# Kernel tuning notes

Hardware: AMD Instinct MI355X
Metric: run time of the kernel (lower is better)

The kernel has to match this reference:

```python
import jax, jax.numpy as jnp
import numpy as np

N_NODES = 50000
N_EDGES = 800000
IN_F = 128
OUT_F = 32
HEADS = 4
EDGE_F = 32  # must equal OUT_F for the original module's shapes to broadcast


def setup_inputs() -> dict:
    key = jax.random.key(0)
    k1, k2, k3, k4, k5, k6, k7 = jax.random.split(key, 7)
    h = jax.random.normal(k1, (N_NODES, IN_F), dtype=jnp.float32)
    edge_indices = jax.random.randint(k2, (2, N_EDGES), 0, N_NODES, dtype=jnp.int32)
    edge_attr = jax.random.normal(k3, (N_EDGES, EDGE_F), dtype=jnp.float32)
    # learned parameters (xavier-ish scaling)
    W = jax.random.normal(k4, (IN_F, HEADS * OUT_F), dtype=jnp.float32) * (1.0 / np.sqrt(IN_F))
    a = jax.random.normal(k5, (HEADS, 2 * OUT_F + EDGE_F), dtype=jnp.float32) * 0.1
    eW = jax.random.normal(k6, (EDGE_F, HEADS * OUT_F), dtype=jnp.float32) * (1.0 / np.sqrt(EDGE_F))
    eb = jnp.zeros((HEADS * OUT_F,), dtype=jnp.float32)
    return {"h": h, "edge_indices": edge_indices, "edge_attr": edge_attr,
            "W": W, "a": a, "eW": eW, "eb": eb}


def reference(h, edge_indices, edge_attr, W, a, eW, eb):
    N = h.shape[0]
    H = a.shape[0]
    F = W.shape[1] // H
    row, col = edge_indices[0], edge_indices[1]

    # node / edge projections
    ht = (h @ W).reshape(N, H, F)                       # [N,H,F]
    et = (edge_attr @ eW + eb).reshape(-1, H, F)        # [E,H,F]

    # split attention vector; avoids materializing the [E,H,3F] concat
    a_i, a_j, a_e = a[:, :F], a[:, F:2 * F], a[:, 2 * F:]
    alpha_i = jnp.einsum('nhf,hf->nh', ht, a_i)         # [N,H]
    alpha_j = jnp.einsum('nhf,hf->nh', ht, a_j)         # [N,H]
    e = alpha_i[row] + alpha_j[col] + jnp.einsum('ehf,hf->eh', et, a_e)  # [E,H]
    e = jax.nn.leaky_relu(e, negative_slope=0.2)

    # scatter-softmax over edges grouped by destination (row), global-max stabilized
    e_exp = jnp.exp(e - jnp.max(e))                     # matches torch exp(e - e.max())
    denom = jax.ops.segment_sum(e_exp, row, num_segments=N)  # [N,H]
    att = e_exp / (denom[row] + 1e-8)                   # [E,H]

    # weighted scatter-add aggregation
    hj = ht[col]                                        # [E,H,F]
    h_out = jax.ops.segment_sum(att[:, :, None] * hj, row, num_segments=N)  # [N,H,F]
    h_out = h_out.reshape(N, H * F)                     # concat=True
    h_out = jax.nn.elu(h_out)                           # dropout=0 (eval)
    return h_out, att
```

## Files before the change

kernel.cpp:

```cpp
#include <hip/hip_runtime.h>
#include <hip/hip_bf16.h>
#include <hip/hip_fp16.h>

#define N_NODES 50000
#define N_EDGES 800000
#define IN_F 128
#define OUT_F 32
#define HEADS 4
#define EDGE_F 32
#define HF 128
#define NB 16
#define SB 256
#define NBLK ((N_NODES + SB - 1) / SB)


__global__ void prep_kernel(const float* __restrict__ eW, const float* __restrict__ eb,
                            const float* __restrict__ a,
                            float* __restrict__ w_eff, float* __restrict__ b_eff) {
    int t = threadIdx.x;
    if (t < 128) {
        int k = t >> 2, h = t & 3;
        float s = 0.f;
        #pragma unroll
        for (int f = 0; f < EDGE_F; ++f)
            s = fmaf(eW[k * HF + h * OUT_F + f], a[h * 96 + 2 * OUT_F + f], s);
        w_eff[k * 4 + h] = s;
    } else if (t < 132) {
        int h = t - 128;
        float s = 0.f;
        #pragma unroll
        for (int f = 0; f < EDGE_F; ++f)
            s = fmaf(eb[h * OUT_F + f], a[h * 96 + 2 * OUT_F + f], s);
        b_eff[h] = s;
    }
}

__global__ __launch_bounds__(256) void node_kernel(
        const float* __restrict__ h, const float* __restrict__ W,
        const float* __restrict__ a,
        __hip_bfloat16* __restrict__ ht_bf,
        float* __restrict__ alpha_i, float* __restrict__ alpha_j) {
    int tid = threadIdx.x;
    int g = tid >> 6, lane = tid & 63;
    int n0 = blockIdx.x * NB;
    __shared__ __align__(16) float hs[NB][IN_F];
    {
        const float4* src = (const float4*)(h + (size_t)n0 * IN_F);
        float4* dst = (float4*)(&hs[0][0]);
        dst[tid] = src[tid];
        dst[tid + 256] = src[tid + 256];
    }
    __syncthreads();
    float acc0[4] = {0.f, 0.f, 0.f, 0.f};
    float acc1[4] = {0.f, 0.f, 0.f, 0.f};
    const float2* Wv = (const float2*)W;
    #pragma unroll 8
    for (int k4 = 0; k4 < IN_F / 4; ++k4) {
        float4 hv[4];
        #pragma unroll
        for (int i = 0; i < 4; ++i)
            hv[i] = *(const float4*)&hs[g * 4 + i][k4 * 4];
        #pragma unroll
        for (int kk = 0; kk < 4; ++kk) {
            float2 w = Wv[(k4 * 4 + kk) * 64 + lane];
            #pragma unroll
            for (int i = 0; i < 4; ++i) {
                float hvv = (&hv[i].x)[kk];
                acc0[i] = fmaf(hvv, w.x, acc0[i]);
                acc1[i] = fmaf(hvv, w.y, acc1[i]);
            }
        }
    }
    int hh = lane >> 4;
    int f0 = (2 * lane) & 31;
    float ai0 = a[hh * 96 + f0],      ai1 = a[hh * 96 + f0 + 1];
    float aj0 = a[hh * 96 + 32 + f0], aj1 = a[hh * 96 + 32 + f0 + 1];
    #pragma unroll
    for (int i = 0; i < 4; ++i) {
        int n = n0 + g * 4 + i;
        *(__hip_bfloat162*)(ht_bf + (size_t)n * HF + 2 * lane) =
            __float22bfloat162_rn(make_float2(acc0[i], acc1[i]));
        float pi = fmaf(acc0[i], ai0, acc1[i] * ai1);
        float pj = fmaf(acc0[i], aj0, acc1[i] * aj1);
        #pragma unroll
        for (int s = 8; s > 0; s >>= 1) {
            pi += __shfl_down(pi, s, 16);
            pj += __shfl_down(pj, s, 16);
        }
        if ((lane & 15) == 0) {
            alpha_i[n * 4 + hh] = pi;
            alpha_j[n * 4 + hh] = pj;
        }
    }
}

__global__ __launch_bounds__(256) void count_kernel(const int* __restrict__ row,
                                                    int* __restrict__ deg,
                                                    int* __restrict__ rank) {
    int t = blockIdx.x * 256 + threadIdx.x;
    if (t < N_EDGES / 4) {
        int4 r4 = ((const int4*)row)[t];
        int4 k4;
        k4.x = atomicAdd(&deg[r4.x], 1);
        k4.y = atomicAdd(&deg[r4.y], 1);
        k4.z = atomicAdd(&deg[r4.z], 1);
        k4.w = atomicAdd(&deg[r4.w], 1);
        ((int4*)rank)[t] = k4;
    }
}

__device__ __forceinline__ int block_incl_scan(int v, int lane, int wid, int* wsum) {
    int x = v;
    #pragma unroll
    for (int s = 1; s < 64; s <<= 1) {
        int y = __shfl_up(x, s, 64);
        if (lane >= s) x += y;
    }
    if (lane == 63) wsum[wid] = x;
    __syncthreads();
    int add = 0;
    #pragma unroll
    for (int w = 0; w < 4; ++w) add += (w < wid) ? wsum[w] : 0;
    return x + add;
}

__global__ __launch_bounds__(SB) void scan1_kernel(const int* __restrict__ deg,
                                                   int* __restrict__ row_off,
                                                   int* __restrict__ blk_sums) {
    __shared__ int wsum[4];
    int i = blockIdx.x * SB + threadIdx.x;
    int v = (i < N_NODES) ? deg[i] : 0;
    int incl = block_incl_scan(v, threadIdx.x & 63, threadIdx.x >> 6, wsum);
    if (i < N_NODES) row_off[i] = incl - v;
    if (threadIdx.x == SB - 1) blk_sums[blockIdx.x] = incl;
}

__global__ __launch_bounds__(SB) void scan2_kernel(int* __restrict__ blk_sums,
                                                   int* __restrict__ blk_off,
                                                   int* __restrict__ row_off) {
    __shared__ int wsum[4];
    int t = threadIdx.x;
    int v = (t < NBLK) ? blk_sums[t] : 0;
    int incl = block_incl_scan(v, t & 63, t >> 6, wsum);
    if (t < NBLK) blk_off[t] = incl - v;
    if (t == SB - 1) row_off[N_NODES] = incl;
}

__global__ __launch_bounds__(SB) void scan3_kernel(const int* __restrict__ blk_off,
                                                   int* __restrict__ row_off) {
    int i = blockIdx.x * SB + threadIdx.x;
    if (i < N_NODES)
        row_off[i] += blk_off[blockIdx.x];
}

__global__ __launch_bounds__(256) void edge_kernel(
        const int* __restrict__ row, const int* __restrict__ col,
        const float* __restrict__ ea,
        const float* __restrict__ w_eff, const float* __restrict__ b_eff,
        const float* __restrict__ alpha_i, const float* __restrict__ alpha_j,
        const int* __restrict__ row_off, const int* __restrict__ rank,
        uint4* __restrict__ rec) {
    __shared__ float wsd[128];
    __shared__ float bs[4];
    int t = threadIdx.x;
    if (t < 128) wsd[t] = w_eff[t];
    if (t < 4) bs[t] = b_eff[t];
    __syncthreads();
    int e = blockIdx.x * 256 + t;
    const float4* src = (const float4*)(ea + (size_t)e * EDGE_F);
    float4 ev[8];
    #pragma unroll
    for (int i = 0; i < 8; ++i) ev[i] = src[i];
    int r = row[e], c = col[e];
    int rk = rank[e];
    float4 ai = *(const float4*)(alpha_i + (size_t)r * 4);
    float4 aj = *(const float4*)(alpha_j + (size_t)c * 4);
    float s0 = bs[0], s1 = bs[1], s2 = bs[2], s3 = bs[3];
    #pragma unroll
    for (int i = 0; i < 8; ++i) {
        #pragma unroll
        for (int kk = 0; kk < 4; ++kk) {
            float x = (&ev[i].x)[kk];
            float4 w4 = *(const float4*)&wsd[(i * 4 + kk) * 4];
            s0 = fmaf(x, w4.x, s0);
            s1 = fmaf(x, w4.y, s1);
            s2 = fmaf(x, w4.z, s2);
            s3 = fmaf(x, w4.w, s3);
        }
    }
    float e0 = s0 + ai.x + aj.x;
    float e1 = s1 + ai.y + aj.y;
    float e2 = s2 + ai.z + aj.z;
    float e3 = s3 + ai.w + aj.w;
    e0 = e0 > 0.f ? e0 : 0.2f * e0;
    e1 = e1 > 0.f ? e1 : 0.2f * e1;
    e2 = e2 > 0.f ? e2 : 0.2f * e2;
    e3 = e3 > 0.f ? e3 : 0.2f * e3;
    __half2 p01 = __floats2half2_rn(__expf(e0), __expf(e1));
    __half2 p23 = __floats2half2_rn(__expf(e2), __expf(e3));
    uint4 out;
    out.x = *reinterpret_cast<unsigned int*>(&p01);
    out.y = *reinterpret_cast<unsigned int*>(&p23);
    out.z = (unsigned int)c;
    out.w = (unsigned int)e;
    int pos = row_off[r] + rk;
    rec[pos] = out;
}

__global__ __launch_bounds__(256) void agg_kernel(
        const int* __restrict__ row_off, const uint4* __restrict__ rec,
        const __hip_bfloat16* __restrict__ ht_bf,
        float* __restrict__ hout, float* __restrict__ att) {
    int wave = threadIdx.x >> 6;
    int lane = threadIdx.x & 63;
    int n = blockIdx.x * 4 + wave;
    if (n >= N_NODES) return;
    int beg = row_off[n], end = row_off[n + 1];
    int h2 = lane >> 4;
    int sh = (h2 & 1) * 16;
    float2 acc0 = {0.f, 0.f}, acc1 = {0.f, 0.f};
    float den0 = 0.f, den1 = 0.f;
    int p = beg;
    for (; p + 1 < end; p += 2) {
        uint4 rA = rec[p];
        uint4 rB = rec[p + 1];
        unsigned int wA = (h2 & 2) ? rA.y : rA.x;
        unsigned int wB = (h2 & 2) ? rB.y : rB.x;
        float exA = __half2float(__ushort_as_half((unsigned short)(wA >> sh)));
        float exB = __half2float(__ushort_as_half((unsigned short)(wB >> sh)));
        int cA = (int)rA.z;
        int cB = (int)rB.z;
        float2 hvA = __bfloat1622float2(
            *(const __hip_bfloat162*)(ht_bf + (size_t)cA * HF + 2 * lane));
        float2 hvB = __bfloat1622float2(
            *(const __hip_bfloat162*)(ht_bf + (size_t)cB * HF + 2 * lane));
        acc0.x = fmaf(exA, hvA.x, acc0.x); acc0.y = fmaf(exA, hvA.y, acc0.y);
        acc1.x = fmaf(exB, hvB.x, acc1.x); acc1.y = fmaf(exB, hvB.y, acc1.y);
        den0 += exA; den1 += exB;
    }
    if (p < end) {
        uint4 rA = rec[p];
        unsigned int wA = (h2 & 2) ? rA.y : rA.x;
        float exA = __half2float(__ushort_as_half((unsigned short)(wA >> sh)));
        int cA = (int)rA.z;
        float2 hvA = __bfloat1622float2(
            *(const __hip_bfloat162*)(ht_bf + (size_t)cA * HF + 2 * lane));
        acc0.x = fmaf(exA, hvA.x, acc0.x); acc0.y = fmaf(exA, hvA.y, acc0.y);
        den0 += exA;
    }
    float den = den0 + den1;
    float rden = 1.0f / (den + 1e-8f);
    float ox = (acc0.x + acc1.x) * rden, oy = (acc0.y + acc1.y) * rden;
    ox = ox > 0.f ? ox : expm1f(ox);
    oy = oy > 0.f ? oy : expm1f(oy);
    float2 o = {ox, oy};
    ((float2*)(hout + (size_t)n * HF))[lane] = o;
    int h = lane & 3;
    float rden_h = __shfl(rden, h * 16, 64);
    for (int p0 = beg; p0 < end; p0 += 16) {
        int q = p0 + (lane >> 2);
        if (q < end) {
            uint4 rQ = rec[q];
            unsigned int w = (h & 2) ? rQ.y : rQ.x;
            float ex = __half2float(__ushort_as_half((unsigned short)(w >> ((h & 1) * 16))));
            att[(size_t)rQ.w * 4 + h] = ex * rden_h;
        }
    }
}

extern "C" void kernel_launch(void* const* d_in, const int* in_sizes, int n_in,
                              void* d_out, int out_size, void* d_ws, size_t ws_size,
                              hipStream_t stream) {
    const float* h  = (const float*)d_in[0];
    const int*   ei = (const int*)  d_in[1];
    const float* ea = (const float*)d_in[2];
    const float* W  = (const float*)d_in[3];
    const float* a  = (const float*)d_in[4];
    const float* eW = (const float*)d_in[5];
    const float* eb = (const float*)d_in[6];

    float* out  = (float*)d_out;
    float* hout = out;
    float* att  = out + (size_t)N_NODES * HF;

    char* wsb = (char*)d_ws;
    __hip_bfloat16* ht_bf = (__hip_bfloat16*)wsb;
    float* alpha_i = (float*)(wsb + (size_t)N_NODES * HF * 2);
    float* alpha_j = alpha_i + N_NODES * HEADS;
    float* w_eff   = alpha_j + N_NODES * HEADS;
    float* b_eff   = w_eff + 128;
    int*   deg     = (int*)(b_eff + 4);
    int*   row_off = deg + N_NODES;
    int*   blk_sums= row_off + N_NODES + 1;
    int*   blk_off = blk_sums + NBLK;
    int*   rank    = (int*)((((uintptr_t)(blk_off + NBLK)) + 15) & ~(uintptr_t)15);
    uint4* rec     = (uint4*)((((uintptr_t)(rank + N_EDGES)) + 15) & ~(uintptr_t)15);

    const int* row = ei;
    const int* col = ei + N_EDGES;

    hipMemsetAsync(deg, 0, (size_t)N_NODES * sizeof(int), stream);

    prep_kernel<<<1, 160, 0, stream>>>(eW, eb, a, w_eff, b_eff);
    node_kernel<<<N_NODES / NB, 256, 0, stream>>>(h, W, a, ht_bf, alpha_i, alpha_j);
    count_kernel<<<(N_EDGES / 4 + 255) / 256, 256, 0, stream>>>(row, deg, rank);
    scan1_kernel<<<NBLK, SB, 0, stream>>>(deg, row_off, blk_sums);
    scan2_kernel<<<1, SB, 0, stream>>>(blk_sums, blk_off, row_off);
    scan3_kernel<<<NBLK, SB, 0, stream>>>(blk_off, row_off);
    edge_kernel<<<N_EDGES / 256, 256, 0, stream>>>(row, col, ea, w_eff, b_eff,
                                                   alpha_i, alpha_j, row_off, rank, rec);
    agg_kernel<<<(N_NODES + 3) / 4, 256, 0, stream>>>(row_off, rec, ht_bf, hout, att);
}
```

Baseline: 378.9 us.

## Use bf16 MFMA with split hi/lo inputs for node projection; stage edge attrs in LDS

Moves the node projection h@W from scalar FMA to 16x16x32 bf16 MFMA. W is pre-transposed and converted to bf16 in a new small kernel, and h is split into bf16 hi and lo parts to recover most of the fp32 accuracy. Both are stored in swizzled LDS tiles, and alpha_i/alpha_j are reduced from the MFMA output layout. The edge kernel now stages edge_attr through padded shared memory so global loads are coalesced. The costs are an extra kernel launch, larger LDS use that lowers occupancy, and reduced precision of W compared with fp32.

```diff
diff --git a/kernel.cpp b/kernel.cpp
--- a/kernel.cpp
+++ b/kernel.cpp
@@ -9,10 +9,20 @@
 #define HEADS 4
 #define EDGE_F 32
 #define HF 128
-#define NB 16
 #define SB 256
 #define NBLK ((N_NODES + SB - 1) / SB)
 
+typedef __attribute__((ext_vector_type(8))) short short8_t;
+typedef __attribute__((ext_vector_type(4))) float f32x4;
+
+__device__ __forceinline__ unsigned short f2bf(float x) {
+    unsigned int u = __float_as_uint(x);
+    unsigned int r = (u + 0x7FFF + ((u >> 16) & 1)) >> 16;
+    return (unsigned short)r;
+}
+__device__ __forceinline__ float bf2f(unsigned short b) {
+    return __uint_as_float(((unsigned int)b) << 16);
+}
 
 __global__ void prep_kernel(const float* __restrict__ eW, const float* __restrict__ eb,
                             const float* __restrict__ a,
@@ -35,62 +45,119 @@
     }
 }
 
+__global__ __launch_bounds__(256) void prepW_kernel(const float* __restrict__ W,
+                                                    unsigned short* __restrict__ W_T) {
+    int g = blockIdx.x * 256 + threadIdx.x;
+    int n = g >> 4, c = g & 15;
+    unsigned short w8[8];
+    #pragma unroll
+    for (int q = 0; q < 8; ++q)
+        w8[q] = f2bf(W[(size_t)(8 * c + q) * 128 + n]);
+    *(uint4*)&W_T[n * 128 + ((c ^ (n & 7)) << 3)] = *(uint4*)w8;
+}
+
 __global__ __launch_bounds__(256) void node_kernel(
-        const float* __restrict__ h, const float* __restrict__ W,
+        const float* __restrict__ h, const unsigned short* __restrict__ W_T,
         const float* __restrict__ a,
         __hip_bfloat16* __restrict__ ht_bf,
         float* __restrict__ alpha_i, float* __restrict__ alpha_j) {
-    int tid = threadIdx.x;
-    int g = tid >> 6, lane = tid & 63;
-    int n0 = blockIdx.x * NB;
-    __shared__ __align__(16) float hs[NB][IN_F];
+    __shared__ __align__(16) unsigned short Wl[128 * 128];
+    __shared__ __align__(16) unsigned short Hhi[64 * 128];
+    __shared__ __align__(16) unsigned short Hlo[64 * 128];
+    int t = threadIdx.x;
+    int lane = t & 63, wave = t >> 6;
+    int nb = blockIdx.x * 64;
     {
-        const float4* src = (const float4*)(h + (size_t)n0 * IN_F);
-        float4* dst = (float4*)(&hs[0][0]);
-        dst[tid] = src[tid];
-        dst[tid + 256] = src[tid + 256];
+        const uint4* src = (const uint4*)W_T;
+        uint4* dst = (uint4*)Wl;
+        #pragma unroll
+        for (int u = 0; u < 8; ++u) dst[t + u * 256] = src[t + u * 256];
+    }
+    #pragma unroll
+    for (int u = 0; u < 8; ++u) {
+        int f = u * 256 + t;
+        int row = f >> 5, q = f & 31;
+        int gn = nb + row; if (gn > N_NODES - 1) gn = N_NODES - 1;
+        float4 v = ((const float4*)h)[(size_t)gn * 32 + q];
+        unsigned short hi[4], lo[4];
+        #pragma unroll
+        for (int x = 0; x < 4; ++x) {
+            float xv = (&v.x)[x];
+            unsigned short hb = f2bf(xv);
+            hi[x] = hb;
+            lo[x] = f2bf(xv - bf2f(hb));
+        }
+        int c = q >> 1, half = q & 1;
+        int off = row * 128 + ((c ^ (row & 7)) << 3) + half * 4;
+        *(uint2*)&Hhi[off] = *(uint2*)hi;
+        *(uint2*)&Hlo[off] = *(uint2*)lo;
     }
     __syncthreads();
-    float acc0[4] = {0.f, 0.f, 0.f, 0.f};
-    float acc1[4] = {0.f, 0.f, 0.f, 0.f};
-    const float2* Wv = (const float2*)W;
-    #pragma unroll 8
-    for (int k4 = 0; k4 < IN_F / 4; ++k4) {
-        float4 hv[4];
-        #pragma unroll
-        for (int i = 0; i < 4; ++i)
-            hv[i] = *(const float4*)&hs[g * 4 + i][k4 * 4];
-        #pragma unroll
-        for (int kk = 0; kk < 4; ++kk) {
-            float2 w = Wv[(k4 * 4 + kk) * 64 + lane];
+    int n0 = nb + wave * 16;
+    if (n0 >= N_NODES) return;
+    int r = lane & 15, g = lane >> 4;
+    short8_t ahi[4], alo[4];
+    #pragma unroll
+    for (int k = 0; k < 4; ++k) {
+        int c = k * 4 + g;
+        int off = (wave * 16 + r) * 128 + ((c ^ (r & 7)) << 3);
+        ahi[k] = *(const short8_t*)&Hhi[off];
+        alo[k] = *(const short8_t*)&Hlo[off];
+    }
+    f32x4 acc[8];
+    #pragma unroll
+    for (int i = 0; i < 8; ++i) acc[i] = (f32x4){0.f, 0.f, 0.f, 0.f};
+    #pragma unroll
+    for (int tt = 0; tt < 8; ++tt) {
+        int n = tt * 16 + r;
+        #pragma unroll
+        for (int k = 0; k < 4; ++k) {
+            int c = k * 4 + g;
+            short8_t b = *(const short8_t*)&Wl[n * 128 + ((c ^ (n & 7)) << 3)];
+            acc[tt] = __builtin_amdgcn_mfma_f32_16x16x32_bf16(ahi[k], b, acc[tt], 0, 0, 0);
+            acc[tt] = __builtin_amdgcn_mfma_f32_16x16x32_bf16(alo[k], b, acc[tt], 0, 0, 0);
+        }
+    }
+    #pragma unroll
+    for (int tt = 0; tt < 8; ++tt)
+        #pragma unroll
+        for (int reg = 0; reg < 4; ++reg) {
+            int rowg = n0 + 4 * g + reg;
+            ((unsigned short*)ht_bf)[(size_t)rowg * 128 + tt * 16 + r] = f2bf(acc[tt][reg]);
+        }
+    float pi[4][4], pj[4][4];
+    #pragma unroll
+    for (int hh = 0; hh < 4; ++hh) {
+        float ai0 = a[hh * 96 + r],      ai1 = a[hh * 96 + 16 + r];
+        float aj0 = a[hh * 96 + 32 + r], aj1 = a[hh * 96 + 48 + r];
+        #pragma unroll
+        for (int reg = 0; reg < 4; ++reg) {
+            float v0 = acc[2 * hh][reg], v1 = acc[2 * hh + 1][reg];
+            pi[hh][reg] = fmaf(v0, ai0, v1 * ai1);
+            pj[hh][reg] = fmaf(v0, aj0, v1 * aj1);
+        }
+    }
+    #pragma unroll
+    for (int hh = 0; hh < 4; ++hh)
+        #pragma unroll
+        for (int reg = 0; reg < 4; ++reg) {
+            float vi = pi[hh][reg], vj = pj[hh][reg];
             #pragma unroll
-            for (int i = 0; i < 4; ++i) {
-                float hvv = (&hv[i].x)[kk];
-                acc0[i] = fmaf(hvv, w.x, acc0[i]);
-                acc1[i] = fmaf(hvv, w.y, acc1[i]);
+            for (int s = 1; s < 16; s <<= 1) {
+                vi += __shfl_xor(vi, s, 64);
+                vj += __shfl_xor(vj, s, 64);
             }
-        }
-    }
-    int hh = lane >> 4;
-    int f0 = (2 * lane) & 31;
-    float ai0 = a[hh * 96 + f0],      ai1 = a[hh * 96 + f0 + 1];
-    float aj0 = a[hh * 96 + 32 + f0], aj1 = a[hh * 96 + 32 + f0 + 1];
-    #pragma unroll
-    for (int i = 0; i < 4; ++i) {
-        int n = n0 + g * 4 + i;
-        *(__hip_bfloat162*)(ht_bf + (size_t)n * HF + 2 * lane) =
-            __float22bfloat162_rn(make_float2(acc0[i], acc1[i]));
-        float pi = fmaf(acc0[i], ai0, acc1[i] * ai1);
-        float pj = fmaf(acc0[i], aj0, acc1[i] * aj1);
-        #pragma unroll
-        for (int s = 8; s > 0; s >>= 1) {
-            pi += __shfl_down(pi, s, 16);
-            pj += __shfl_down(pj, s, 16);
-        }
-        if ((lane & 15) == 0) {
-            alpha_i[n * 4 + hh] = pi;
-            alpha_j[n * 4 + hh] = pj;
-        }
+            pi[hh][reg] = vi; pj[hh][reg] = vj;
+        }
+    if (r == 0) {
+        #pragma unroll
+        for (int hh = 0; hh < 4; ++hh)
+            #pragma unroll
+            for (int reg = 0; reg < 4; ++reg) {
+                int rowg = n0 + 4 * g + reg;
+                alpha_i[rowg * 4 + hh] = pi[hh][reg];
+                alpha_j[rowg * 4 + hh] = pj[hh][reg];
+            }
     }
 }
 
@@ -160,17 +227,27 @@
         const float* __restrict__ alpha_i, const float* __restrict__ alpha_j,
         const int* __restrict__ row_off, const int* __restrict__ rank,
         uint4* __restrict__ rec) {
+    __shared__ __align__(16) float eas[256 * 36];
     __shared__ float wsd[128];
     __shared__ float bs[4];
     int t = threadIdx.x;
     if (t < 128) wsd[t] = w_eff[t];
     if (t < 4) bs[t] = b_eff[t];
+    int e0 = blockIdx.x * 256;
+    {
+        const float4* src = (const float4*)ea + (size_t)e0 * 8;
+        #pragma unroll
+        for (int u = 0; u < 8; ++u) {
+            int f = u * 256 + t;
+            int el = f >> 3, j = f & 7;
+            *(float4*)&eas[el * 36 + 4 * j] = src[f];
+        }
+    }
     __syncthreads();
-    int e = blockIdx.x * 256 + t;
-    const float4* src = (const float4*)(ea + (size_t)e * EDGE_F);
+    int e = e0 + t;
     float4 ev[8];
     #pragma unroll
-    for (int i = 0; i < 8; ++i) ev[i] = src[i];
+    for (int i = 0; i < 8; ++i) ev[i] = *(const float4*)&eas[t * 36 + 4 * i];
     int r = row[e], c = col[e];
     int rk = rank[e];
     float4 ai = *(const float4*)(alpha_i + (size_t)r * 4);
@@ -188,16 +265,16 @@
             s3 = fmaf(x, w4.w, s3);
         }
     }
-    float e0 = s0 + ai.x + aj.x;
-    float e1 = s1 + ai.y + aj.y;
-    float e2 = s2 + ai.z + aj.z;
-    float e3 = s3 + ai.w + aj.w;
-    e0 = e0 > 0.f ? e0 : 0.2f * e0;
-    e1 = e1 > 0.f ? e1 : 0.2f * e1;
-    e2 = e2 > 0.f ? e2 : 0.2f * e2;
-    e3 = e3 > 0.f ? e3 : 0.2f * e3;
-    __half2 p01 = __floats2half2_rn(__expf(e0), __expf(e1));
-    __half2 p23 = __floats2half2_rn(__expf(e2), __expf(e3));
+    float e0v = s0 + ai.x + aj.x;
+    float e1v = s1 + ai.y + aj.y;
+    float e2v = s2 + ai.z + aj.z;
+    float e3v = s3 + ai.w + aj.w;
+    e0v = e0v > 0.f ? e0v : 0.2f * e0v;
+    e1v = e1v > 0.f ? e1v : 0.2f * e1v;
+    e2v = e2v > 0.f ? e2v : 0.2f * e2v;
+    e3v = e3v > 0.f ? e3v : 0.2f * e3v;
+    __half2 p01 = __floats2half2_rn(__expf(e0v), __expf(e1v));
+    __half2 p23 = __floats2half2_rn(__expf(e2v), __expf(e3v));
     uint4 out;
     out.x = *reinterpret_cast<unsigned int*>(&p01);
     out.y = *reinterpret_cast<unsigned int*>(&p23);
@@ -289,7 +366,8 @@
     float* alpha_j = alpha_i + N_NODES * HEADS;
     float* w_eff   = alpha_j + N_NODES * HEADS;
     float* b_eff   = w_eff + 128;
-    int*   deg     = (int*)(b_eff + 4);
+    unsigned short* W_T = (unsigned short*)(b_eff + 4);
+    int*   deg     = (int*)(W_T + 128 * 128);
     int*   row_off = deg + N_NODES;
     int*   blk_sums= row_off + N_NODES + 1;
     int*   blk_off = blk_sums + NBLK;
@@ -302,7 +380,8 @@
     hipMemsetAsync(deg, 0, (size_t)N_NODES * sizeof(int), stream);
 
     prep_kernel<<<1, 160, 0, stream>>>(eW, eb, a, w_eff, b_eff);
-    node_kernel<<<N_NODES / NB, 256, 0, stream>>>(h, W, a, ht_bf, alpha_i, alpha_j);
+    prepW_kernel<<<8, 256, 0, stream>>>(W, W_T);
+    node_kernel<<<(N_NODES + 63) / 64, 256, 0, stream>>>(h, W_T, a, ht_bf, alpha_i, alpha_j);
     count_kernel<<<(N_EDGES / 4 + 255) / 256, 256, 0, stream>>>(row, deg, rank);
     scan1_kernel<<<NBLK, SB, 0, stream>>>(deg, row_off, blk_sums);
     scan2_kernel<<<1, SB, 0, stream>>>(blk_sums, blk_off, row_off);
```

Measured after the change: 337.2 us. 11.0% less time.
